# Kernel optimization log

Hardware: AMD Instinct MI355X
Metric: run time of the kernel (lower is better)

## Reference

```python
import jax, jax.numpy as jnp
import numpy as np

MB = 512          # mini_batch_size from init
BETA = 0.5        # RKHSMatrixOptimizer beta
N_SIGMAS = 50     # forward calls sigma_optimizer.step(..., 50)
EPS = 1e-6        # epsilon added to eigenvalues


def _pdist2(a):
    # squared Euclidean pairwise distances, matches torch.cdist(a, a)**2
    sq = jnp.sum(a * a, axis=1)
    d2 = sq[:, None] + sq[None, :] - 2.0 * (a @ a.T)
    return jnp.maximum(d2, 0.0)


def _rbf(d2, sigma):
    return jnp.exp(-d2 / (sigma ** 2))


def _entropy(A):
    # matrix-based Renyi entropy: eigh, +eps, -sum(w log2 w)
    w = jnp.linalg.eigvalsh(A) + EPS
    return -jnp.sum(w * jnp.log2(w))


def _joint_entropy(Ax, Ay):
    aux = Ax * Ay
    return _entropy(aux / jnp.trace(aux))


def _mi(Ax, Ay):
    return _entropy(Ax) + _entropy(Ay) - _joint_entropy(Ax, Ay)


def setup_inputs() -> dict:
    key = jax.random.key(0)
    k1, k2, k3 = jax.random.split(key, 3)
    x = jax.random.normal(k1, (4096, 8192), dtype=jnp.float32)
    inp = jax.random.normal(k2, (4096, 3, 32, 32), dtype=jnp.float32)
    label = jax.random.uniform(k3, (4096, 10), dtype=jnp.float32)
    return {"x": x, "input": inp, "label": label}


def reference(x, input, label):
    xf = x.reshape(x.shape[0], -1)
    inpf = input.reshape(input.shape[0], -1)
    n_batches = xf.shape[0] // MB

    sigma = None
    Ixt, Ity = [], []
    for b in range(n_batches):
        sl = slice(b * MB, (b + 1) * MB)
        xb, ib, lb = xf[sl], inpf[sl], label[sl]
        n = xb.shape[0]

        # label kernel Ky = RBF(label_batch, 0.1)
        Ky = _rbf(_pdist2(lb), 0.1)

        # sigma search: compute pairwise distances ONCE, broadcast over 50 sigmas
        d2 = _pdist2(xb)
        d = jnp.sqrt(d2)
        mean_d = jnp.sum(d) / jnp.maximum(jnp.sum(d2 > 0), 1)  # mean of nonzero dists
        start = 0.1 * mean_d
        step = (10.0 * mean_d - start) / N_SIGMAS
        sigmas = start + step * jnp.arange(N_SIGMAS, dtype=jnp.float32)  # np.arange equiv
        Ks = jnp.exp(-d2[None, :, :] / (sigmas[:, None, None] ** 2))  # [50, n, n]
        num = jnp.sum(Ks * Ky[None], axis=(1, 2))
        den = jnp.sqrt(jnp.sum(Ks * Ks, axis=(1, 2))) * jnp.linalg.norm(Ky)
        loss = num / den  # kernel alignment
        sigma_t = sigmas[jnp.argmax(loss)]
        sigma = sigma_t if sigma is None else BETA * sigma + (1.0 - BETA) * sigma_t

        # normalized Gram matrices (tensorRBFMatrix divides by batch size)
        A = _rbf(d2, sigma) / n
        Ay = Ky / n
        Ax = _rbf(_pdist2(ib), 8.0) / n

        Ixt.append(_mi(Ax, A))
        Ity.append(_mi(A, Ay))

    Ixt_mean = jnp.mean(jnp.stack(Ixt))
    Ity_mean = jnp.mean(jnp.stack(Ity))
    # torch forward returns x unchanged; MI values are stored as side effects.
    return x, Ixt_mean, Ity_mean
```

## Files before the change

### kernel.cpp

```cpp
#include <hip/hip_runtime.h>
#include <hip/hip_bf16.h>
#include <math.h>


#define NBATCH 8
#define MBS    512
#define DXX    8192
#define DII    3072
#define NSIG   50
#define NN     262144
#define NTOT   ((size_t)33554432)
#define NGEMM  576

#define I_SUMD  0
#define I_KYF   8
#define I_SIGMA 24
#define I_ENT   32
#define I_NUM   96
#define I_DEN   512
#define I_AX2   912
#define I_A2    920
#define I_JX2   928
#define I_JY2   936

typedef __attribute__((ext_vector_type(8))) short bf16x8;
typedef __attribute__((ext_vector_type(4))) float f32x4;

__device__ __forceinline__ size_t slotOf(int b, int m) {
  return ((size_t)(b * 5 + m)) * (size_t)NN;
}

__device__ __forceinline__ short f2b(float f) {
  __hip_bfloat16 h = __float2bfloat16(f);
  return *(short*)&h;
}

__device__ __forceinline__ ushort4 cvt4(float4 a) {
  ushort4 v;
  v.x = (ushort)f2b(a.x); v.y = (ushort)f2b(a.y);
  v.z = (ushort)f2b(a.z); v.w = (ushort)f2b(a.w);
  return v;
}

__device__ __forceinline__ double n4(float4 a) {
  return (double)a.x * a.x + (double)a.y * a.y + (double)a.z * a.z + (double)a.w * a.w;
}

__global__ void k_copy(const float4* __restrict__ src, float4* __restrict__ dst, size_t n4) {
  size_t i = (size_t)blockIdx.x * blockDim.x + threadIdx.x;
  size_t stride = (size_t)gridDim.x * blockDim.x;
  for (; i < n4; i += stride) dst[i] = src[i];
}

__global__ __launch_bounds__(256) void k_prep(
    const float4* __restrict__ x4,
    const float* __restrict__ inp, const float* __restrict__ lab,
    ushort* __restrict__ xbf, ushort* __restrict__ inpbf,
    float* __restrict__ nrmx, float* __restrict__ nrmi,
    float* __restrict__ eig, double* __restrict__ scal)
{
  __shared__ double red[256];
  int bid = blockIdx.x, t = threadIdx.x;

  if (bid < 4096) {
    int row = bid;
    const float4* p4 = x4 + (size_t)row * 2048;
    float4 f0 = p4[t];
    float4 f1 = p4[t + 256];
    float4 f2 = p4[t + 512];
    float4 f3 = p4[t + 768];
    float4 f4 = p4[t + 1024];
    float4 f5 = p4[t + 1280];
    float4 f6 = p4[t + 1536];
    float4 f7 = p4[t + 1792];
    __builtin_amdgcn_sched_barrier(0);
    ushort4* o4 = (ushort4*)(xbf + (size_t)row * 8192);
    o4[t]        = cvt4(f0);
    o4[t + 256]  = cvt4(f1);
    o4[t + 512]  = cvt4(f2);
    o4[t + 768]  = cvt4(f3);
    o4[t + 1024] = cvt4(f4);
    o4[t + 1280] = cvt4(f5);
    o4[t + 1536] = cvt4(f6);
    o4[t + 1792] = cvt4(f7);
    double s = n4(f0) + n4(f1) + n4(f2) + n4(f3) + n4(f4) + n4(f5) + n4(f6) + n4(f7);
    red[t] = s; __syncthreads();
    for (int o2 = 128; o2 > 0; o2 >>= 1) {
      if (t < o2) red[t] += red[t + o2];
      __syncthreads();
    }
    if (t == 0) nrmx[row] = (float)red[0];
    return;
  }

  if (bid < 6144) {
    int p = bid - 4096;
    const float4* src4 = (const float4*)inp + (size_t)p * 768;
    ushort4* dst4 = (ushort4*)inpbf + (size_t)p * 768;
    float4 g0 = src4[t];
    float4 g1 = src4[t + 256];
    float4 g2 = src4[t + 512];
    __builtin_amdgcn_sched_barrier(0);
    dst4[t]       = cvt4(g0);
    dst4[t + 256] = cvt4(g1);
    dst4[t + 512] = cvt4(g2);
    double s0 = n4(g0), s1 = n4(g2);
    double sm = n4(g1);
    if (t < 128) s0 += sm; else s1 += sm;
    red[t] = s0; __syncthreads();
    for (int o = 128; o > 0; o >>= 1) { if (t < o) red[t] += red[t + o]; __syncthreads(); }
    if (t == 0) nrmi[2 * p] = (float)red[0];
    __syncthreads();
    red[t] = s1; __syncthreads();
    for (int o = 128; o > 0; o >>= 1) { if (t < o) red[t] += red[t + o]; __syncthreads(); }
    if (t == 0) nrmi[2 * p + 1] = (float)red[0];
    return;
  }

  int idx = bid - 6144;
  int b = idx >> 8, xb = idx & 255;
  int e0 = xb * 1024 + t * 4;
  int i = e0 >> 9;
  const float* L = lab + (size_t)b * MBS * 10;
  float4 out;
  double s = 0.0;
#pragma unroll
  for (int u = 0; u < 4; u++) {
    int j = (e0 & 511) + u;
    float d2 = 0.0f;
#pragma unroll
    for (int d = 0; d < 10; d++) { float dd = L[i * 10 + d] - L[j * 10 + d]; d2 += dd * dd; }
    float ky = __expf(-d2 * 100.0f);
    ((float*)&out)[u] = ky * (1.0f / 512.0f);
    s += (double)ky * ky;
  }
  *(float4*)&eig[slotOf(b, 2) + e0] = out;
  red[t] = s; __syncthreads();
  for (int o = 128; o > 0; o >>= 1) { if (t < o) red[t] += red[t + o]; __syncthreads(); }
  if (t == 0) atomicAdd(&scal[I_KYF + b], red[0]);
}

#define LSTR 72
#define LGKM0_BAR                                                             \
  do {                                                                        \
    asm volatile("s_waitcnt lgkmcnt(0)" ::: "memory");                        \
    __builtin_amdgcn_s_barrier();                                             \
    __builtin_amdgcn_sched_barrier(0);                                        \
  } while (0)

#define LOAD_SET(A0, A1, B0, B1, K0)                                          \
  do {                                                                        \
    A0 = *(const bf16x8*)&srcA0[K0];                                          \
    A1 = *(const bf16x8*)&srcA1[K0];                                          \
    B0 = *(const bf16x8*)&srcB0[K0];                                          \
    B1 = *(const bf16x8*)&srcB1[K0];                                          \
  } while (0)

#define WRITE_LDS(BUF, A0, A1, B0, B1)                                        \
  do {                                                                        \
    *(bf16x8*)&As[BUF][rr * LSTR + cc] = A0;                                  \
    *(bf16x8*)&As[BUF][(32 + rr) * LSTR + cc] = A1;                           \
    *(bf16x8*)&Bs[BUF][rr * LSTR + cc] = B0;                                  \
    *(bf16x8*)&Bs[BUF][(32 + rr) * LSTR + cc] = B1;                           \
  } while (0)

#define MFMA_PHASE(BUF)                                                       \
  do {                                                                        \
    _Pragma("unroll")                                                         \
    for (int ks = 0; ks < 2; ks++) {                                          \
      bf16x8 af0 = *(const bf16x8*)&As[BUF][(wr + l15) * LSTR + ks * 32 + l4 * 8];          \
      bf16x8 af1 = *(const bf16x8*)&As[BUF][(wr + 16 + l15) * LSTR + ks * 32 + l4 * 8];     \
      bf16x8 bg0 = *(const bf16x8*)&Bs[BUF][(wc + l15) * LSTR + ks * 32 + l4 * 8];          \
      bf16x8 bg1 = *(const bf16x8*)&Bs[BUF][(wc + 16 + l15) * LSTR + ks * 32 + l4 * 8];     \
      acc00 = __builtin_amdgcn_mfma_f32_16x16x32_bf16(af0, bg0, acc00, 0, 0, 0);            \
      acc01 = __builtin_amdgcn_mfma_f32_16x16x32_bf16(af0, bg1, acc01, 0, 0, 0);            \
      acc10 = __builtin_amdgcn_mfma_f32_16x16x32_bf16(af1, bg0, acc10, 0, 0, 0);            \
      acc11 = __builtin_amdgcn_mfma_f32_16x16x32_bf16(af1, bg1, acc11, 0, 0, 0);            \
    }                                                                         \
  } while (0)

__global__ __launch_bounds__(256) void k_gemm2(
    const ushort* __restrict__ xbf, const ushort* __restrict__ inpbf,
    const float* __restrict__ nrmx, const float* __restrict__ nrmi,
    float* __restrict__ eig, double* __restrict__ scal,
    unsigned long long* __restrict__ cnt,
    const f32x4* __restrict__ xsrc, f32x4* __restrict__ xdst)
{
  int id = blockIdx.x;
  int tid = threadIdx.x;

  if (id >= NGEMM) {
    size_t base = (size_t)(id - NGEMM) * 4096 + tid;
#pragma unroll
    for (int h = 0; h < 2; h++) {
      size_t o = base + (size_t)h * 2048;
      f32x4 c0 = __builtin_nontemporal_load(xsrc + o);
      f32x4 c1 = __builtin_nontemporal_load(xsrc + o + 256);
      f32x4 c2 = __builtin_nontemporal_load(xsrc + o + 512);
      f32x4 c3 = __builtin_nontemporal_load(xsrc + o + 768);
      f32x4 c4 = __builtin_nontemporal_load(xsrc + o + 1024);
      f32x4 c5 = __builtin_nontemporal_load(xsrc + o + 1280);
      f32x4 c6 = __builtin_nontemporal_load(xsrc + o + 1536);
      f32x4 c7 = __builtin_nontemporal_load(xsrc + o + 1792);
      __builtin_amdgcn_sched_barrier(0);
      __builtin_nontemporal_store(c0, xdst + o);
      __builtin_nontemporal_store(c1, xdst + o + 256);
      __builtin_nontemporal_store(c2, xdst + o + 512);
      __builtin_nontemporal_store(c3, xdst + o + 768);
      __builtin_nontemporal_store(c4, xdst + o + 1024);
      __builtin_nontemporal_store(c5, xdst + o + 1280);
      __builtin_nontemporal_store(c6, xdst + o + 1536);
      __builtin_nontemporal_store(c7, xdst + o + 1792);
    }
    return;
  }

  int b = id & 7;
  int tm = id >> 3;
  int mode = (tm >= 36) ? 1 : 0;
  int t = tm - mode * 36;
  int bx = 0;
#pragma unroll
  for (int r = 1; r < 8; r++) if (t >= (r * (r + 1)) / 2) bx = r;
  int by = t - (bx * (bx + 1)) / 2;
  bool diag = (bx == by);
  int D = mode ? DII : DXX;
  const ushort* src = (mode ? inpbf : xbf) + (size_t)b * MBS * D;
  const float* nb = (mode ? nrmi : nrmx) + b * MBS;
  int row0 = bx * 64, col0 = by * 64;

  __shared__ ushort As[2][64 * LSTR];
  __shared__ ushort Bs[2][64 * LSTR];
  __shared__ double redd[256];
  __shared__ unsigned redi[256];

  int lane = tid & 63, w = tid >> 6;
  int wr = (w >> 1) * 32, wc = (w & 1) * 32;
  int l15 = lane & 15, l4 = lane >> 4;

  f32x4 acc00 = {0.f, 0.f, 0.f, 0.f}, acc01 = {0.f, 0.f, 0.f, 0.f};
  f32x4 acc10 = {0.f, 0.f, 0.f, 0.f}, acc11 = {0.f, 0.f, 0.f, 0.f};

  int rr = tid >> 3;
  int cc = (tid & 7) * 8;

  const ushort* srcA0 = src + (size_t)(row0 + rr) * D + cc;
  const ushort* srcA1 = src + (size_t)(row0 + 32 + rr) * D + cc;
  const ushort* srcB0 = src + (size_t)(col0 + rr) * D + cc;
  const ushort* srcB1 = src + (size_t)(col0 + 32 + rr) * D + cc;

  bf16x8 pa0, pa1, pb0, pb1;
  bf16x8 qa0, qa1, qb0, qb1;

  LOAD_SET(pa0, pa1, pb0, pb1, 0);
  LOAD_SET(qa0, qa1, qb0, qb1, 64);

  int nk = D >> 6;
  for (int k = 0; k < nk; k += 2) {
    WRITE_LDS(0, pa0, pa1, pb0, pb1);
    if (k + 2 < nk) LOAD_SET(pa0, pa1, pb0, pb1, (k + 2) << 6);
    LGKM0_BAR;
    MFMA_PHASE(0);
    WRITE_LDS(1, qa0, qa1, qb0, qb1);
    if (k + 3 < nk) LOAD_SET(qa0, qa1, qb0, qb1, (k + 3) << 6);
    LGKM0_BAR;
    MFMA_PHASE(1);
  }

  float* dst = eig + slotOf(b, mode ? 0 : 1);
  double lsum = 0.0; unsigned lcnt = 0;
#define EPI(ACC, M, N)                                                        \
  do {                                                                        \
    int gr = row0 + wr + (M) * 16 + l4 * 4;                                   \
    int gc = col0 + wc + (N) * 16 + l15;                                      \
    float nj = nb[gc];                                                        \
    _Pragma("unroll")                                                         \
    for (int v = 0; v < 4; v++) {                                             \
      int gi = gr + v;                                                        \
      float d2 = nb[gi] + nj - 2.0f * ACC[v];                                 \
      d2 = fmaxf(d2, 0.0f);                                                   \
      if (gi == gc) d2 = 0.0f;                                                \
      float val;                                                              \
      if (mode == 0) {                                                        \
        val = d2;                                                             \
        if (d2 > 0.0f) { lsum += (double)sqrtf(d2); lcnt++; }                 \
      } else {                                                                \
        val = __expf(-d2 * (1.0f / 64.0f)) * (1.0f / 512.0f);                 \
        lsum += (double)val * val;                                            \
      }                                                                       \
      dst[(size_t)gi * MBS + gc] = val;                                       \
      if (!diag) dst[(size_t)gc * MBS + gi] = val;                            \
    }                                                                         \
  } while (0)
  EPI(acc00, 0, 0); EPI(acc01, 0, 1); EPI(acc10, 1, 0); EPI(acc11, 1, 1);
#undef EPI

  if (!diag) { lsum *= 2.0; lcnt *= 2; }
  __syncthreads();
  redd[tid] = lsum; redi[tid] = lcnt; __syncthreads();
  for (int o = 128; o > 0; o >>= 1) {
    if (tid < o) { redd[tid] += redd[tid + o]; redi[tid] += redi[tid + o]; }
    __syncthreads();
  }
  if (tid == 0) {
    if (mode == 0) {
      atomicAdd(&scal[I_SUMD + b], redd[0]);
      atomicAdd(&cnt[b], (unsigned long long)redi[0]);
    } else {
      atomicAdd(&scal[I_AX2 + b], redd[0]);
    }
  }
}

__global__ __launch_bounds__(256) void k_loss(const float* __restrict__ eig,
                                              double* __restrict__ scal,
                                              const unsigned long long* __restrict__ cnt,
                                              unsigned* __restrict__ done) {
  int b = blockIdx.z, g = blockIdx.y;
  double c = (double)cnt[b]; if (c < 1.0) c = 1.0;
  float md = (float)(scal[I_SUMD + b] / c);
  const float4* d2p = (const float4*)(eig + slotOf(b, 1));
  const float4* ayp = (const float4*)(eig + slotOf(b, 2));
  float inv[25], ln[25], ld[25];
#pragma unroll
  for (int i = 0; i < 25; i++) {
    float sg = md * (0.1f + 0.198f * (float)(g * 25 + i));
    inv[i] = 1.0f / (sg * sg);
    ln[i] = 0.0f; ld[i] = 0.0f;
  }
  int base = blockIdx.x * 2048 + threadIdx.x;
#pragma unroll
  for (int l = 0; l < 8; l++) {
    float4 d2v = d2p[base + l * 256];
    float4 ayv = ayp[base + l * 256];
#pragma unroll
    for (int u = 0; u < 4; u++) {
      float d2 = ((const float*)&d2v)[u];
      float ay = ((const float*)&ayv)[u];
#pragma unroll
      for (int i = 0; i < 25; i++) {
        float kk = __expf(-d2 * inv[i]);
        ln[i] = fmaf(kk, ay, ln[i]);
        ld[i] = fmaf(kk, kk, ld[i]);
      }
    }
  }
#pragma unroll
  for (int i = 0; i < 25; i++) {
    float a = ln[i], d = ld[i];
    for (int o = 32; o > 0; o >>= 1) {
      a += __shfl_down(a, o, 64);
      d += __shfl_down(d, o, 64);
    }
    if ((threadIdx.x & 63) == 0) {
      atomicAdd(&scal[I_NUM + b * NSIG + g * 25 + i], (double)a * 512.0);
      atomicAdd(&scal[I_DEN + b * NSIG + g * 25 + i], (double)d);
    }
  }
  __syncthreads();
  if (threadIdx.x == 0) {
    __threadfence();
    unsigned r = atomicAdd(done, 1u);
    if (r == 32 * 2 * NBATCH - 1) {
      __threadfence();
      double sigma = 0.0;
      for (int bb = 0; bb < NBATCH; bb++) {
        double cc2 = (double)cnt[bb]; if (cc2 < 1.0) cc2 = 1.0;
        double mdd = scal[I_SUMD + bb] / cc2;
        double kyf = sqrt(scal[I_KYF + bb]);
        double best = -1.0; int bi = 0;
        for (int s = 0; s < NSIG; s++) {
          double num = scal[I_NUM + bb * NSIG + s];
          double den = sqrt(scal[I_DEN + bb * NSIG + s]) * kyf;
          double loss = num / den;
          if (loss > best) { best = loss; bi = s; }
        }
        double st = mdd * (0.1 + 0.198 * (double)bi);
        sigma = (bb == 0) ? st : 0.5 * sigma + 0.5 * st;
        scal[I_SIGMA + bb] = sigma;
      }
    }
  }
}

__global__ __launch_bounds__(256) void k_aj(float* __restrict__ eig,
                                            double* __restrict__ scal) {
  int b = blockIdx.y;
  float sg = (float)scal[I_SIGMA + b];
  float inv = 1.0f / (sg * sg);
  float* A        = eig + slotOf(b, 1);
  const float* AX = eig + slotOf(b, 0);
  const float* AY = eig + slotOf(b, 2);
  float* J1       = eig + slotOf(b, 3);
  float* J2       = eig + slotOf(b, 4);
  double s1 = 0.0, s2 = 0.0, s3 = 0.0;
  size_t base = (size_t)blockIdx.x * 2048 + (size_t)threadIdx.x * 8;
#pragma unroll
  for (int h = 0; h < 2; h++) {
    size_t e = base + h * 4;
    float4 d2v = *(float4*)&A[e];
    float4 axv = *(const float4*)&AX[e];
    float4 ayv = *(const float4*)&AY[e];
    float4 av, j1v, j2v;
#pragma unroll
    for (int u = 0; u < 4; u++) {
      float a = __expf(-((const float*)&d2v)[u] * inv) * (1.0f / 512.0f);
      float j1 = ((const float*)&axv)[u] * a;
      float j2 = a * ((const float*)&ayv)[u];
      ((float*)&av)[u] = a; ((float*)&j1v)[u] = j1; ((float*)&j2v)[u] = j2;
      s1 += (double)a * a; s2 += (double)j1 * j1; s3 += (double)j2 * j2;
    }
    *(float4*)&A[e] = av;
    *(float4*)&J1[e] = j1v;
    *(float4*)&J2[e] = j2v;
  }
  __shared__ double r1[256], r2[256], r3[256];
  r1[threadIdx.x] = s1; r2[threadIdx.x] = s2; r3[threadIdx.x] = s3;
  __syncthreads();
  for (int o = 128; o > 0; o >>= 1) {
    if (threadIdx.x < o) {
      r1[threadIdx.x] += r1[threadIdx.x + o];
      r2[threadIdx.x] += r2[threadIdx.x + o];
      r3[threadIdx.x] += r3[threadIdx.x + o];
    }
    __syncthreads();
  }
  if (threadIdx.x == 0) {
    atomicAdd(&scal[I_A2 + b], r1[0]);
    atomicAdd(&scal[I_JX2 + b], r2[0]);
    atomicAdd(&scal[I_JY2 + b], r3[0]);
  }
}

__global__ __launch_bounds__(512) void k_eigen(float* __restrict__ eig,
                                               double* __restrict__ scal,
                                               unsigned* __restrict__ done,
                                               float* __restrict__ out) {
  int blk = blockIdx.x; int b = blk / 5, m = blk % 5;
  int t = threadIdx.x;
  double off2, scale0;
  if (m == 0)      { off2 = scal[I_AX2 + b] - (1.0 / 512.0);              scale0 = 1.0; }
  else if (m == 1) { off2 = scal[I_A2 + b]  - (1.0 / 512.0);              scale0 = 1.0; }
  else if (m == 2) { off2 = (scal[I_KYF + b] - 512.0) * (1.0 / 262144.0); scale0 = 1.0; }
  else if (m == 3) { off2 = scal[I_JX2 + b] - 7.450580596923828125e-9;    scale0 = 512.0; }
  else             { off2 = scal[I_JY2 + b] - 7.450580596923828125e-9;    scale0 = 512.0; }

  if (off2 * scale0 * scale0 <= 1e-8) {
    if (t == 0) {
      double diagv = (m >= 3) ? (1.0 / 262144.0) : (1.0 / 512.0);
      double wv = diagv * scale0 + 1e-6;
      scal[I_ENT + b * 5 + m] = -512.0 * wv * log2(wv);
    }
  } else {
    float* M = eig + slotOf(b, m);
    __shared__ double red[512];
    __shared__ float csA[256], csB[256];
    __shared__ int anyrot;
    __shared__ double sh_scale, sh_off2;

    red[t] = (double)M[(size_t)t * 513]; __syncthreads();
    for (int o = 256; o > 0; o >>= 1) { if (t < o) red[t] += red[t + o]; __syncthreads(); }
    if (t == 0) { double trace = red[0]; sh_scale = (m >= 3) ? 1.0 / trace : 1.0; }
    __syncthreads();
    double scale = sh_scale;

    for (int sweep = 0; sweep < 30; sweep++) {
      double c2 = 0.0;
      for (int i = 0; i < 512; i++) {
        if (i != t) { float v = M[(size_t)i * 512 + t]; c2 += (double)v * v; }
      }
      red[t] = c2; __syncthreads();
      for (int o = 256; o > 0; o >>= 1) { if (t < o) red[t] += red[t + o]; __syncthreads(); }
      if (t == 0) sh_off2 = red[0];
      __syncthreads();
      if (sh_off2 * scale * scale <= 1e-8) break;

      for (int r = 0; r < 511; r++) {
        if (t == 0) anyrot = 0;
        __syncthreads();
        if (t < 256) {
          int p, q;
          if (t == 0) { p = 511; q = r; }
          else { p = (r + t) % 511; q = (r + 511 - t) % 511; }
          float app = M[(size_t)p * 512 + p];
          float aqq = M[(size_t)q * 512 + q];
          float apq = M[(size_t)p * 512 + q];
          float c = 1.0f, sr = 0.0f;
          if (fabsf(apq) > 1e-12f) {
            float th = (aqq - app) / (2.0f * apq);
            float tt = ((th >= 0.0f) ? 1.0f : -1.0f) / (fabsf(th) + sqrtf(1.0f + th * th));
            c = 1.0f / sqrtf(1.0f + tt * tt);
            sr = tt * c;
            anyrot = 1;
          }
          csA[t] = c; csB[t] = sr;
        }
        __syncthreads();
        if (anyrot) {
          int pair = t >> 1, half = t & 1;
          float c = csA[pair], sr = csB[pair];
          int p, q;
          if (pair == 0) { p = 511; q = r; }
          else { p = (r + pair) % 511; q = (r + 511 - pair) % 511; }
          if (sr != 0.0f) {
            size_t rp = (size_t)p * 512, rq = (size_t)q * 512;
            int j0 = half * 256;
            for (int j = j0; j < j0 + 256; j++) {
              float xx = M[rp + j], yy = M[rq + j];
              M[rp + j] = c * xx - sr * yy;
              M[rq + j] = sr * xx + c * yy;
            }
          }
          __syncthreads();
          if (sr != 0.0f) {
            int j0 = half * 256;
            for (int j = j0; j < j0 + 256; j++) {
              float xx = M[(size_t)j * 512 + p], yy = M[(size_t)j * 512 + q];
              M[(size_t)j * 512 + p] = c * xx - sr * yy;
              M[(size_t)j * 512 + q] = sr * xx + c * yy;
            }
          }
        }
        __syncthreads();
      }
    }

    double wv = (double)M[(size_t)t * 513] * scale + 1e-6;
    red[t] = -wv * log2(wv); __syncthreads();
    for (int o = 256; o > 0; o >>= 1) { if (t < o) red[t] += red[t + o]; __syncthreads(); }
    if (t == 0) scal[I_ENT + b * 5 + m] = red[0];
  }

  __syncthreads();
  if (t == 0) {
    __threadfence();
    unsigned r = atomicAdd(done, 1u);
    if (r == 39) {
      __threadfence();
      double ixt = 0.0, ity = 0.0;
      for (int bb = 0; bb < NBATCH; bb++) {
        const double* E = &scal[I_ENT + bb * 5];
        ixt += E[0] + E[1] - E[3];
        ity += E[1] + E[2] - E[4];
      }
      out[NTOT]     = (float)(ixt / 8.0);
      out[NTOT + 1] = (float)(ity / 8.0);
    }
  }
}

extern "C" void kernel_launch(void* const* d_in, const int* in_sizes, int n_in,
                              void* d_out, int out_size, void* d_ws, size_t ws_size,
                              hipStream_t stream) {
  const float* x   = (const float*)d_in[0];
  const float* inp = (const float*)d_in[1];
  const float* lab = (const float*)d_in[2];
  float* out = (float*)d_out;

  char* ws = (char*)d_ws;
  double* scal = (double*)ws;
  unsigned long long* cnt = (unsigned long long*)(ws + 7552);
  unsigned* done_loss = (unsigned*)(ws + 7616);
  unsigned* done_eig  = (unsigned*)(ws + 7620);
  float* nrmx = (float*)(ws + 7680);
  float* nrmi = (float*)(ws + 24064);

  const size_t EIG_OFF = 65536;
  bool big = ws_size >= EIG_OFF + 134217728ULL;
  char* base = big ? (ws + EIG_OFF) : (char*)d_out;
  float* eig = (float*)base;
  ushort* xbf = (ushort*)(base + 41943040);
  ushort* inpbf = (ushort*)(base + 109051904);

  hipMemsetAsync(ws, 0, 7624, stream);

  k_prep<<<8192, 256, 0, stream>>>((const float4*)x, inp, lab,
                                   xbf, inpbf, nrmx, nrmi, eig, scal);
  int ncopy = big ? 2048 : 0;
  k_gemm2<<<NGEMM + ncopy, 256, 0, stream>>>(xbf, inpbf, nrmx, nrmi, eig, scal, cnt,
                                             (const f32x4*)x, (f32x4*)d_out);
  k_loss<<<dim3(32, 2, NBATCH), 256, 0, stream>>>(eig, scal, cnt, done_loss);
  k_aj<<<dim3(128, NBATCH), 256, 0, stream>>>(eig, scal);
  k_eigen<<<40, 512, 0, stream>>>(eig, scal, done_eig, out);
  if (!big) {
    k_copy<<<2048, 256, 0, stream>>>((const float4*)x, (float4*)d_out, NTOT / 4);
  }
}
```

Baseline: 281.7 us.

## Interleave copy blocks with GEMM blocks, widen K tile to 128, raise MFMA priority

```diff
diff --git a/kernel.cpp b/kernel.cpp
--- a/kernel.cpp
+++ b/kernel.cpp
@@ -140,7 +140,7 @@
   if (t == 0) atomicAdd(&scal[I_KYF + b], red[0]);
 }
 
-#define LSTR 72
+#define LSTR2 136
 #define LGKM0_BAR                                                             \
   do {                                                                        \
     asm volatile("s_waitcnt lgkmcnt(0)" ::: "memory");                        \
@@ -148,35 +148,45 @@
     __builtin_amdgcn_sched_barrier(0);                                        \
   } while (0)
 
-#define LOAD_SET(A0, A1, B0, B1, K0)                                          \
+#define LOAD_SET(A0, A1, A2, A3, B0, B1, B2, B3, K0)                          \
   do {                                                                        \
     A0 = *(const bf16x8*)&srcA0[K0];                                          \
     A1 = *(const bf16x8*)&srcA1[K0];                                          \
+    A2 = *(const bf16x8*)&srcA2[K0];                                          \
+    A3 = *(const bf16x8*)&srcA3[K0];                                          \
     B0 = *(const bf16x8*)&srcB0[K0];                                          \
     B1 = *(const bf16x8*)&srcB1[K0];                                          \
+    B2 = *(const bf16x8*)&srcB2[K0];                                          \
+    B3 = *(const bf16x8*)&srcB3[K0];                                          \
   } while (0)
 
-#define WRITE_LDS(BUF, A0, A1, B0, B1)                                        \
+#define WRITE_LDS(BUF, A0, A1, A2, A3, B0, B1, B2, B3)                        \
   do {                                                                        \
-    *(bf16x8*)&As[BUF][rr * LSTR + cc] = A0;                                  \
-    *(bf16x8*)&As[BUF][(32 + rr) * LSTR + cc] = A1;                           \
-    *(bf16x8*)&Bs[BUF][rr * LSTR + cc] = B0;                                  \
-    *(bf16x8*)&Bs[BUF][(32 + rr) * LSTR + cc] = B1;                           \
+    *(bf16x8*)&As[BUF][rr2 * LSTR2 + cc2] = A0;                               \
+    *(bf16x8*)&As[BUF][(16 + rr2) * LSTR2 + cc2] = A1;                        \
+    *(bf16x8*)&As[BUF][(32 + rr2) * LSTR2 + cc2] = A2;                        \
+    *(bf16x8*)&As[BUF][(48 + rr2) * LSTR2 + cc2] = A3;                        \
+    *(bf16x8*)&Bs[BUF][rr2 * LSTR2 + cc2] = B0;                               \
+    *(bf16x8*)&Bs[BUF][(16 + rr2) * LSTR2 + cc2] = B1;                        \
+    *(bf16x8*)&Bs[BUF][(32 + rr2) * LSTR2 + cc2] = B2;                        \
+    *(bf16x8*)&Bs[BUF][(48 + rr2) * LSTR2 + cc2] = B3;                        \
   } while (0)
 
 #define MFMA_PHASE(BUF)                                                       \
   do {                                                                        \
+    __builtin_amdgcn_s_setprio(1);                                            \
     _Pragma("unroll")                                                         \
-    for (int ks = 0; ks < 2; ks++) {                                          \
-      bf16x8 af0 = *(const bf16x8*)&As[BUF][(wr + l15) * LSTR + ks * 32 + l4 * 8];          \
-      bf16x8 af1 = *(const bf16x8*)&As[BUF][(wr + 16 + l15) * LSTR + ks * 32 + l4 * 8];     \
-      bf16x8 bg0 = *(const bf16x8*)&Bs[BUF][(wc + l15) * LSTR + ks * 32 + l4 * 8];          \
-      bf16x8 bg1 = *(const bf16x8*)&Bs[BUF][(wc + 16 + l15) * LSTR + ks * 32 + l4 * 8];     \
-      acc00 = __builtin_amdgcn_mfma_f32_16x16x32_bf16(af0, bg0, acc00, 0, 0, 0);            \
-      acc01 = __builtin_amdgcn_mfma_f32_16x16x32_bf16(af0, bg1, acc01, 0, 0, 0);            \
-      acc10 = __builtin_amdgcn_mfma_f32_16x16x32_bf16(af1, bg0, acc10, 0, 0, 0);            \
-      acc11 = __builtin_amdgcn_mfma_f32_16x16x32_bf16(af1, bg1, acc11, 0, 0, 0);            \
+    for (int ks = 0; ks < 4; ks++) {                                          \
+      bf16x8 af0 = *(const bf16x8*)&As[BUF][(wr + l15) * LSTR2 + ks * 32 + l4 * 8];          \
+      bf16x8 af1 = *(const bf16x8*)&As[BUF][(wr + 16 + l15) * LSTR2 + ks * 32 + l4 * 8];     \
+      bf16x8 bg0 = *(const bf16x8*)&Bs[BUF][(wc + l15) * LSTR2 + ks * 32 + l4 * 8];          \
+      bf16x8 bg1 = *(const bf16x8*)&Bs[BUF][(wc + 16 + l15) * LSTR2 + ks * 32 + l4 * 8];     \
+      acc00 = __builtin_amdgcn_mfma_f32_16x16x32_bf16(af0, bg0, acc00, 0, 0, 0);             \
+      acc01 = __builtin_amdgcn_mfma_f32_16x16x32_bf16(af0, bg1, acc01, 0, 0, 0);             \
+      acc10 = __builtin_amdgcn_mfma_f32_16x16x32_bf16(af1, bg0, acc10, 0, 0, 0);             \
+      acc11 = __builtin_amdgcn_mfma_f32_16x16x32_bf16(af1, bg1, acc11, 0, 0, 0);             \
     }                                                                         \
+    __builtin_amdgcn_s_setprio(0);                                            \
   } while (0)
 
 __global__ __launch_bounds__(256) void k_gemm2(
@@ -184,39 +194,46 @@
     const float* __restrict__ nrmx, const float* __restrict__ nrmi,
     float* __restrict__ eig, double* __restrict__ scal,
     unsigned long long* __restrict__ cnt,
-    const f32x4* __restrict__ xsrc, f32x4* __restrict__ xdst)
+    const f32x4* __restrict__ xsrc, f32x4* __restrict__ xdst, int inter)
 {
   int id = blockIdx.x;
   int tid = threadIdx.x;
 
-  if (id >= NGEMM) {
-    size_t base = (size_t)(id - NGEMM) * 4096 + tid;
-#pragma unroll
-    for (int h = 0; h < 2; h++) {
-      size_t o = base + (size_t)h * 2048;
-      f32x4 c0 = __builtin_nontemporal_load(xsrc + o);
-      f32x4 c1 = __builtin_nontemporal_load(xsrc + o + 256);
-      f32x4 c2 = __builtin_nontemporal_load(xsrc + o + 512);
-      f32x4 c3 = __builtin_nontemporal_load(xsrc + o + 768);
-      f32x4 c4 = __builtin_nontemporal_load(xsrc + o + 1024);
-      f32x4 c5 = __builtin_nontemporal_load(xsrc + o + 1280);
-      f32x4 c6 = __builtin_nontemporal_load(xsrc + o + 1536);
-      f32x4 c7 = __builtin_nontemporal_load(xsrc + o + 1792);
-      __builtin_amdgcn_sched_barrier(0);
-      __builtin_nontemporal_store(c0, xdst + o);
-      __builtin_nontemporal_store(c1, xdst + o + 256);
-      __builtin_nontemporal_store(c2, xdst + o + 512);
-      __builtin_nontemporal_store(c3, xdst + o + 768);
-      __builtin_nontemporal_store(c4, xdst + o + 1024);
-      __builtin_nontemporal_store(c5, xdst + o + 1280);
-      __builtin_nontemporal_store(c6, xdst + o + 1536);
-      __builtin_nontemporal_store(c7, xdst + o + 1792);
-    }
-    return;
-  }
-
-  int b = id & 7;
-  int tm = id >> 3;
+  int gid;
+  if (inter) {
+    int g = id / 41, r = id % 41;
+    if (r >= 9) {
+      size_t base = (size_t)(g * 32 + (r - 9)) * 4096 + tid;
+#pragma unroll
+      for (int h = 0; h < 2; h++) {
+        size_t o = base + (size_t)h * 2048;
+        f32x4 c0 = __builtin_nontemporal_load(xsrc + o);
+        f32x4 c1 = __builtin_nontemporal_load(xsrc + o + 256);
+        f32x4 c2 = __builtin_nontemporal_load(xsrc + o + 512);
+        f32x4 c3 = __builtin_nontemporal_load(xsrc + o + 768);
+        f32x4 c4 = __builtin_nontemporal_load(xsrc + o + 1024);
+        f32x4 c5 = __builtin_nontemporal_load(xsrc + o + 1280);
+        f32x4 c6 = __builtin_nontemporal_load(xsrc + o + 1536);
+        f32x4 c7 = __builtin_nontemporal_load(xsrc + o + 1792);
+        __builtin_amdgcn_sched_barrier(0);
+        __builtin_nontemporal_store(c0, xdst + o);
+        __builtin_nontemporal_store(c1, xdst + o + 256);
+        __builtin_nontemporal_store(c2, xdst + o + 512);
+        __builtin_nontemporal_store(c3, xdst + o + 768);
+        __builtin_nontemporal_store(c4, xdst + o + 1024);
+        __builtin_nontemporal_store(c5, xdst + o + 1280);
+        __builtin_nontemporal_store(c6, xdst + o + 1536);
+        __builtin_nontemporal_store(c7, xdst + o + 1792);
+      }
+      return;
+    }
+    gid = g * 9 + r;
+  } else {
+    gid = id;
+  }
+
+  int b = gid & 7;
+  int tm = gid >> 3;
   int mode = (tm >= 36) ? 1 : 0;
   int t = tm - mode * 36;
   int bx = 0;
@@ -229,8 +246,8 @@
   const float* nb = (mode ? nrmi : nrmx) + b * MBS;
   int row0 = bx * 64, col0 = by * 64;
 
-  __shared__ ushort As[2][64 * LSTR];
-  __shared__ ushort Bs[2][64 * LSTR];
+  __shared__ ushort As[2][64 * LSTR2];
+  __shared__ ushort Bs[2][64 * LSTR2];
   __shared__ double redd[256];
   __shared__ unsigned redi[256];
 
@@ -241,28 +258,32 @@
   f32x4 acc00 = {0.f, 0.f, 0.f, 0.f}, acc01 = {0.f, 0.f, 0.f, 0.f};
   f32x4 acc10 = {0.f, 0.f, 0.f, 0.f}, acc11 = {0.f, 0.f, 0.f, 0.f};
 
-  int rr = tid >> 3;
-  int cc = (tid & 7) * 8;
-
-  const ushort* srcA0 = src + (size_t)(row0 + rr) * D + cc;
-  const ushort* srcA1 = src + (size_t)(row0 + 32 + rr) * D + cc;
-  const ushort* srcB0 = src + (size_t)(col0 + rr) * D + cc;
-  const ushort* srcB1 = src + (size_t)(col0 + 32 + rr) * D + cc;
-
-  bf16x8 pa0, pa1, pb0, pb1;
-  bf16x8 qa0, qa1, qb0, qb1;
-
-  LOAD_SET(pa0, pa1, pb0, pb1, 0);
-  LOAD_SET(qa0, qa1, qb0, qb1, 64);
-
-  int nk = D >> 6;
+  int rr2 = tid >> 4;
+  int cc2 = (tid & 15) * 8;
+
+  const ushort* srcA0 = src + (size_t)(row0 + rr2) * D + cc2;
+  const ushort* srcA1 = src + (size_t)(row0 + 16 + rr2) * D + cc2;
+  const ushort* srcA2 = src + (size_t)(row0 + 32 + rr2) * D + cc2;
+  const ushort* srcA3 = src + (size_t)(row0 + 48 + rr2) * D + cc2;
+  const ushort* srcB0 = src + (size_t)(col0 + rr2) * D + cc2;
+  const ushort* srcB1 = src + (size_t)(col0 + 16 + rr2) * D + cc2;
+  const ushort* srcB2 = src + (size_t)(col0 + 32 + rr2) * D + cc2;
+  const ushort* srcB3 = src + (size_t)(col0 + 48 + rr2) * D + cc2;
+
+  bf16x8 pa0, pa1, pa2, pa3, pb0, pb1, pb2, pb3;
+  bf16x8 qa0, qa1, qa2, qa3, qb0, qb1, qb2, qb3;
+
+  LOAD_SET(pa0, pa1, pa2, pa3, pb0, pb1, pb2, pb3, 0);
+  LOAD_SET(qa0, qa1, qa2, qa3, qb0, qb1, qb2, qb3, 128);
+
+  int nk = D >> 7;
   for (int k = 0; k < nk; k += 2) {
-    WRITE_LDS(0, pa0, pa1, pb0, pb1);
-    if (k + 2 < nk) LOAD_SET(pa0, pa1, pb0, pb1, (k + 2) << 6);
+    WRITE_LDS(0, pa0, pa1, pa2, pa3, pb0, pb1, pb2, pb3);
+    if (k + 2 < nk) LOAD_SET(pa0, pa1, pa2, pa3, pb0, pb1, pb2, pb3, (k + 2) << 7);
     LGKM0_BAR;
     MFMA_PHASE(0);
-    WRITE_LDS(1, qa0, qa1, qb0, qb1);
-    if (k + 3 < nk) LOAD_SET(qa0, qa1, qb0, qb1, (k + 3) << 6);
+    WRITE_LDS(1, qa0, qa1, qa2, qa3, qb0, qb1, qb2, qb3);
+    if (k + 3 < nk) LOAD_SET(qa0, qa1, qa2, qa3, qb0, qb1, qb2, qb3, (k + 3) << 7);
     LGKM0_BAR;
     MFMA_PHASE(1);
   }
@@ -576,9 +597,9 @@
 
   k_prep<<<8192, 256, 0, stream>>>((const float4*)x, inp, lab,
                                    xbf, inpbf, nrmx, nrmi, eig, scal);
-  int ncopy = big ? 2048 : 0;
-  k_gemm2<<<NGEMM + ncopy, 256, 0, stream>>>(xbf, inpbf, nrmx, nrmi, eig, scal, cnt,
-                                             (const f32x4*)x, (f32x4*)d_out);
+  int nblk = big ? 2624 : NGEMM;
+  k_gemm2<<<nblk, 256, 0, stream>>>(xbf, inpbf, nrmx, nrmi, eig, scal, cnt,
+                                    (const f32x4*)x, (f32x4*)d_out, big ? 1 : 0);
   k_loss<<<dim3(32, 2, NBATCH), 256, 0, stream>>>(eig, scal, cnt, done_loss);
   k_aj<<<dim3(128, NBATCH), 256, 0, stream>>>(eig, scal);
   k_eigen<<<40, 512, 0, stream>>>(eig, scal, done_eig, out);
```

After: 267.1 us. 5.2% less time.
